# Kernel tuning notes

Measured on AMD Instinct MI355X. Metric: run time of the kernel, lower is better.

## Reference

```python
import jax, jax.numpy as jnp
import numpy as np

N_EXPERTS = 8
D_MODEL = 1024
D_FF = 2048
N_TOKENS = 4096
TOP_K = 2


def _init_expert_weight(key, shape):
    # matches torch init: bound = sqrt(3) * (sqrt(1/3)/sqrt(fan_in)) = 1/sqrt(fan_in)
    fan_in = shape[1]
    bound = 1.0 / np.sqrt(fan_in)
    return jax.random.uniform(key, shape, dtype=jnp.float32, minval=-bound, maxval=bound)


def setup_inputs() -> dict:
    key = jax.random.key(0)
    k_x, k_idx, k_w, k1, k2, k3 = jax.random.split(key, 6)
    x = jax.random.normal(k_x, (N_TOKENS, D_MODEL), dtype=jnp.float32)
    expert_indices = jax.random.randint(k_idx, (N_TOKENS, TOP_K), 0, N_EXPERTS)
    expert_weights = jax.random.uniform(k_w, (N_TOKENS, TOP_K), dtype=jnp.float32)
    w1 = _init_expert_weight(k1, (N_EXPERTS, D_MODEL, D_FF))
    w2 = _init_expert_weight(k2, (N_EXPERTS, D_MODEL, D_FF))
    w3 = _init_expert_weight(k3, (N_EXPERTS, D_FF, D_MODEL))
    return {"x": x, "expert_indices": expert_indices, "expert_weights": expert_weights,
            "w1": w1, "w2": w2, "w3": w3}


def reference(x, expert_indices, expert_weights, w1, w2, w3):
    # SwiGLU per expert, computed densely over all (token, expert) pairs,
    # then the top-k selected expert outputs are gathered and combined.
    # Mathematically identical to the padded-bmm dispatch/combine in the source.
    gate = jax.nn.silu(jnp.einsum('td,edf->tef', x, w1))   # [T, E, F]
    value = jnp.einsum('td,edf->tef', x, w2)               # [T, E, F]
    hidden = gate * value                                  # [T, E, F]
    out_e = jnp.einsum('tef,efd->ted', hidden, w3)         # [T, E, D]
    # gather each token's top-k expert outputs: [T, K, D]
    sel = jnp.take_along_axis(out_e, expert_indices[:, :, None], axis=1)
    return jnp.sum(sel * expert_weights[:, :, None], axis=1)  # [T, D]
```

## Files before the change

kernel.cpp:

```cpp
#include <hip/hip_runtime.h>
#include <hip/hip_bf16.h>

#define N_TOK   4096
#define DM      1024
#define DF      2048
#define NEXP    8
#define NPAIR   (N_TOK * 2)
#define BM      128
#define BN      128
#define BK      32

typedef __attribute__((ext_vector_type(8))) short bf16x8;
typedef __attribute__((ext_vector_type(4))) float f32x4;

__device__ __forceinline__ unsigned short to_bf16(float f) {
    unsigned u = __builtin_bit_cast(unsigned, f);
    unsigned r = (u + 0x7FFFu + ((u >> 16) & 1u)) >> 16;
    return (unsigned short)r;
}
__device__ __forceinline__ unsigned pk_bf16(float a, float b) {
    return (unsigned)to_bf16(a) | ((unsigned)to_bf16(b) << 16);
}
__device__ __forceinline__ void gld16(const unsigned short* g, unsigned short* l) {
    __builtin_amdgcn_global_load_lds(
        (const __attribute__((address_space(1))) unsigned int*)(g),
        (__attribute__((address_space(3))) unsigned int*)(l), 16, 0, 0);
}

__global__ __launch_bounds__(1024)
void k_sort(const int* __restrict__ eidx, int* __restrict__ meta,
            int* __restrict__ rows) {
    __shared__ int cnt[NEXP];
    __shared__ int cur[NEXP];
    const int tid = threadIdx.x;
    if (tid < NEXP) cnt[tid] = 0;
    __syncthreads();
    #pragma unroll
    for (int i = tid; i < NPAIR; i += 1024) atomicAdd(&cnt[eidx[i] & 7], 1);
    __syncthreads();
    if (tid == 0) {
        int off = 0, mt = 0;
        for (int e = 0; e < NEXP; ++e) {
            meta[16 + e] = off; meta[25 + e] = mt; cur[e] = off;
            int c = cnt[e];
            off += c; mt += (c + BM - 1) / BM;
        }
        meta[16 + NEXP] = off; meta[25 + NEXP] = mt; meta[34] = mt;
    }
    __syncthreads();
    #pragma unroll
    for (int i = tid; i < NPAIR; i += 1024) {
        int e = eidx[i] & 7;
        int p = atomicAdd(&cur[e], 1);
        rows[p] = i;
    }
}

__device__ __forceinline__ void d_transpose(const float* __restrict__ src,
                                            unsigned short* __restrict__ dst,
                                            int K, int F, int e, int bx, int by,
                                            unsigned short* tile, int t) {
    const int k0 = by * 64;
    const int f0 = bx * 64;
    const float* s = src + (size_t)e * K * F;
    unsigned short* d = dst + (size_t)e * K * F;
    const int fi = t & 63;
    const int kg = t >> 6;
    #pragma unroll
    for (int i = 0; i < 16; ++i) {
        int k = kg * 16 + i;
        tile[k * 80 + fi] = to_bf16(s[(size_t)(k0 + k) * F + f0 + fi]);
    }
    __syncthreads();
    const int kc = (t & 7) * 8;
    const int fo = t >> 3;
    #pragma unroll
    for (int j = 0; j < 2; ++j) {
        int f = fo + j * 32;
        unsigned short v[8];
        #pragma unroll
        for (int i = 0; i < 8; ++i) v[i] = tile[(kc + i) * 80 + f];
        uint4 w;
        w.x = (unsigned)v[0] | ((unsigned)v[1] << 16);
        w.y = (unsigned)v[2] | ((unsigned)v[3] << 16);
        w.z = (unsigned)v[4] | ((unsigned)v[5] << 16);
        w.w = (unsigned)v[6] | ((unsigned)v[7] << 16);
        *(uint4*)&d[(size_t)(f0 + f) * K + k0 + kc] = w;
    }
}

__global__ __launch_bounds__(256)
void k_prepass(const float* __restrict__ x, unsigned short* __restrict__ xb,
               const float* __restrict__ w1, unsigned short* __restrict__ w1t,
               const float* __restrict__ w2, unsigned short* __restrict__ w2t,
               const float* __restrict__ w3, unsigned short* __restrict__ w3t) {
    __shared__ __align__(16) unsigned short tile[64 * 80];
    const int b = blockIdx.x;
    const int t = threadIdx.x;
    if (b < 2048) {
        int i = (b * 256 + t) * 8;
        float4 v0 = *(const float4*)(x + i);
        float4 v1 = *(const float4*)(x + i + 4);
        uint4 w;
        w.x = pk_bf16(v0.x, v0.y); w.y = pk_bf16(v0.z, v0.w);
        w.z = pk_bf16(v1.x, v1.y); w.w = pk_bf16(v1.z, v1.w);
        *(uint4*)(xb + i) = w;
    } else if (b < 6144) {
        int l = b - 2048;
        int e = l >> 9, rem = l & 511;
        d_transpose(w1, w1t, DM, DF, e, rem & 31, rem >> 5, tile, t);
    } else if (b < 10240) {
        int l = b - 6144;
        int e = l >> 9, rem = l & 511;
        d_transpose(w2, w2t, DM, DF, e, rem & 31, rem >> 5, tile, t);
    } else {
        int l = b - 10240;
        int e = l >> 9, rem = l & 511;
        d_transpose(w3, w3t, DF, DM, e, rem & 15, rem >> 4, tile, t);
    }
}

__device__ __forceinline__ bool xcd_map(const int* meta, int bid, int ngroups,
                                        int& mt, int& ng) {
    const int MT = meta[34];
    const int x = bid & 7;
    const int j = bid >> 3;
    const int q = MT >> 3, r = MT & 7;
    const int Sx = q + (x < r ? 1 : 0);
    if (Sx == 0 || j >= Sx * ngroups) return false;
    ng = j / Sx;
    const int mtl = j - ng * Sx;
    mt = x * q + (x < r ? x : r) + mtl;
    return true;
}

__global__ __launch_bounds__(256, 2)
void k_gemm1_bf(const unsigned short* __restrict__ xb,
                const unsigned short* __restrict__ w1t,
                const unsigned short* __restrict__ w2t,
                const int* __restrict__ meta,
                const int* __restrict__ rows,
                unsigned short* __restrict__ H)
{
    __shared__ __align__(16) unsigned short As [BM * BK];
    __shared__ __align__(16) unsigned short B1s[BN * BK];
    __shared__ __align__(16) unsigned short B2s[BN * BK];
    __shared__ int s_tok[BM];

    int mt, ng;
    if (!xcd_map(meta, blockIdx.x, DF / BN, mt, ng)) return;
    int e = 0;
    #pragma unroll
    for (int i = 0; i < NEXP - 1; ++i) if (mt >= meta[25 + i + 1]) e = i + 1;
    const int rowEnd = meta[16 + e + 1];
    const int row0   = meta[16 + e] + (mt - meta[25 + e]) * BM;
    const int f0     = ng * BN;
    const int tid    = threadIdx.x;

    if (tid < BM) {
        int gr = row0 + tid;
        s_tok[tid] = (gr < rowEnd) ? (rows[gr] >> 1) : 0;
    }
    __syncthreads();

    const int lane = tid & 63;
    const int wave = tid >> 6;
    const int r0 = wave * 32 + (lane >> 2);
    const int r1 = r0 + 16;
    const int kb = (lane & 3) * 8;
    const unsigned short* a_src0 = xb + (size_t)s_tok[r0] * DM + kb;
    const unsigned short* a_src1 = xb + (size_t)s_tok[r1] * DM + kb;
    const size_t wb = (size_t)e * DM * DF;
    const unsigned short* b1_src0 = w1t + wb + (size_t)(f0 + r0) * DM + kb;
    const unsigned short* b1_src1 = w1t + wb + (size_t)(f0 + r1) * DM + kb;
    const unsigned short* b2_src0 = w2t + wb + (size_t)(f0 + r0) * DM + kb;
    const unsigned short* b2_src1 = w2t + wb + (size_t)(f0 + r1) * DM + kb;
    unsigned short* As0  = &As [wave * 1024];
    unsigned short* As1  = &As [wave * 1024 + 512];
    unsigned short* B1s0 = &B1s[wave * 1024];
    unsigned short* B1s1 = &B1s[wave * 1024 + 512];
    unsigned short* B2s0 = &B2s[wave * 1024];
    unsigned short* B2s1 = &B2s[wave * 1024 + 512];

    f32x4 accg[4][4], accv[4][4];
    #pragma unroll
    for (int i = 0; i < 4; ++i)
        #pragma unroll
        for (int j = 0; j < 4; ++j) { accg[i][j] = (f32x4)0.f; accv[i][j] = (f32x4)0.f; }

    const int wm = (wave >> 1) * 64;
    const int wn = (wave & 1) * 64;
    const int am = lane & 15;
    const int ak = (lane >> 4) * 8;

    for (int k0 = 0; k0 < DM; k0 += BK) {
        gld16(a_src0 + k0, As0);
        gld16(a_src1 + k0, As1);
        gld16(b1_src0 + k0, B1s0);
        gld16(b1_src1 + k0, B1s1);
        gld16(b2_src0 + k0, B2s0);
        gld16(b2_src1 + k0, B2s1);
        __syncthreads();

        bf16x8 a[4], b1[4], b2[4];
        #pragma unroll
        for (int mi = 0; mi < 4; ++mi) a[mi] = *(const bf16x8*)&As[(wm + mi * 16 + am) * BK + ak];
        #pragma unroll
        for (int ni = 0; ni < 4; ++ni) {
            b1[ni] = *(const bf16x8*)&B1s[(wn + ni * 16 + am) * BK + ak];
            b2[ni] = *(const bf16x8*)&B2s[(wn + ni * 16 + am) * BK + ak];
        }
        #pragma unroll
        for (int mi = 0; mi < 4; ++mi)
            #pragma unroll
            for (int ni = 0; ni < 4; ++ni) {
                accg[mi][ni] = __builtin_amdgcn_mfma_f32_16x16x32_bf16(a[mi], b1[ni], accg[mi][ni], 0, 0, 0);
                accv[mi][ni] = __builtin_amdgcn_mfma_f32_16x16x32_bf16(a[mi], b2[ni], accv[mi][ni], 0, 0, 0);
            }
        __syncthreads();
    }

    const int cn = lane & 15;
    const int cq = (lane >> 4) * 4;
    #pragma unroll
    for (int mi = 0; mi < 4; ++mi) {
        #pragma unroll
        for (int r = 0; r < 4; ++r) {
            const int row = wm + mi * 16 + cq + r;
            const int gr  = row0 + row;
            if (gr < rowEnd) {
                unsigned short* dst = H + (size_t)gr * DF + f0 + wn;
                #pragma unroll
                for (int ni = 0; ni < 4; ++ni) {
                    float g = accg[mi][ni][r];
                    float v = accv[mi][ni][r];
                    float h = (g * v) / (1.f + __expf(-g));
                    dst[ni * 16 + cn] = to_bf16(h);
                }
            }
        }
    }
}

__global__ __launch_bounds__(256, 2)
void k_gemm2_bf(const unsigned short* __restrict__ H,
                const unsigned short* __restrict__ w3t,
                const int* __restrict__ meta,
                const int* __restrict__ rows,
                const float* __restrict__ ew,
                float* __restrict__ out)
{
    __shared__ __align__(16) unsigned short As[BM * BK];
    __shared__ __align__(16) unsigned short Bs[BN * BK];
    __shared__ int   s_tok[BM];
    __shared__ float s_w[BM];

    int mt, ng;
    if (!xcd_map(meta, blockIdx.x, DM / BN, mt, ng)) return;
    int e = 0;
    #pragma unroll
    for (int i = 0; i < NEXP - 1; ++i) if (mt >= meta[25 + i + 1]) e = i + 1;
    const int rowEnd = meta[16 + e + 1];
    const int row0   = meta[16 + e] + (mt - meta[25 + e]) * BM;
    const int d0     = ng * BN;
    const int tid    = threadIdx.x;

    if (tid < BM) {
        int gr = row0 + tid;
        if (gr < rowEnd) { int pr = rows[gr]; s_tok[tid] = pr >> 1; s_w[tid] = ew[pr]; }
        else             { s_tok[tid] = 0;    s_w[tid] = 0.f; }
    }
    __syncthreads();

    const int lane = tid & 63;
    const int wave = tid >> 6;
    const int r0 = wave * 32 + (lane >> 2);
    const int r1 = r0 + 16;
    const int kb = (lane & 3) * 8;
    int gr0 = row0 + r0; if (gr0 > NPAIR - 1) gr0 = NPAIR - 1;
    int gr1 = row0 + r1; if (gr1 > NPAIR - 1) gr1 = NPAIR - 1;
    const unsigned short* a_src0 = H + (size_t)gr0 * DF + kb;
    const unsigned short* a_src1 = H + (size_t)gr1 * DF + kb;
    const size_t wb = (size_t)e * DM * DF;
    const unsigned short* b_src0 = w3t + wb + (size_t)(d0 + r0) * DF + kb;
    const unsigned short* b_src1 = w3t + wb + (size_t)(d0 + r1) * DF + kb;
    unsigned short* As0 = &As[wave * 1024];
    unsigned short* As1 = &As[wave * 1024 + 512];
    unsigned short* Bs0 = &Bs[wave * 1024];
    unsigned short* Bs1 = &Bs[wave * 1024 + 512];

    f32x4 acc[4][4];
    #pragma unroll
    for (int i = 0; i < 4; ++i)
        #pragma unroll
        for (int j = 0; j < 4; ++j) acc[i][j] = (f32x4)0.f;

    const int wm = (wave >> 1) * 64;
    const int wn = (wave & 1) * 64;
    const int am = lane & 15;
    const int ak = (lane >> 4) * 8;

    for (int k0 = 0; k0 < DF; k0 += BK) {
        gld16(a_src0 + k0, As0);
        gld16(a_src1 + k0, As1);
        gld16(b_src0 + k0, Bs0);
        gld16(b_src1 + k0, Bs1);
        __syncthreads();

        bf16x8 a[4], b[4];
        #pragma unroll
        for (int mi = 0; mi < 4; ++mi) a[mi] = *(const bf16x8*)&As[(wm + mi * 16 + am) * BK + ak];
        #pragma unroll
        for (int ni = 0; ni < 4; ++ni) b[ni] = *(const bf16x8*)&Bs[(wn + ni * 16 + am) * BK + ak];
        #pragma unroll
        for (int mi = 0; mi < 4; ++mi)
            #pragma unroll
            for (int ni = 0; ni < 4; ++ni)
                acc[mi][ni] = __builtin_amdgcn_mfma_f32_16x16x32_bf16(a[mi], b[ni], acc[mi][ni], 0, 0, 0);
        __syncthreads();
    }

    const int cn = lane & 15;
    const int cq = (lane >> 4) * 4;
    #pragma unroll
    for (int mi = 0; mi < 4; ++mi) {
        #pragma unroll
        for (int r = 0; r < 4; ++r) {
            const int row = wm + mi * 16 + cq + r;
            const int gr  = row0 + row;
            if (gr < rowEnd) {
                const int   tok = s_tok[row];
                const float wgt = s_w[row];
                float* dst = out + (size_t)tok * DM + d0 + wn;
                #pragma unroll
                for (int ni = 0; ni < 4; ++ni)
                    atomicAdd(&dst[ni * 16 + cn], wgt * acc[mi][ni][r]);
            }
        }
    }
}

__global__ __launch_bounds__(256)
void k_fallback(const float* __restrict__ x, const int* __restrict__ eidx,
                const float* __restrict__ ew, const float* __restrict__ w1,
                const float* __restrict__ w2, const float* __restrict__ w3,
                float* __restrict__ out)
{
    __shared__ float xs[DM];
    __shared__ float hs[DF];
    const int pair = blockIdx.x;
    const int t = pair >> 1;
    const int e = eidx[pair] & 7;
    const float wgt = ew[pair];
    const int tid = threadIdx.x;
    for (int i = tid; i < DM; i += 256) xs[i] = x[(size_t)t * DM + i];
    __syncthreads();
    for (int f = tid; f < DF; f += 256) {
        const float* c1 = w1 + (size_t)e * DM * DF + f;
        const float* c2 = w2 + (size_t)e * DM * DF + f;
        float g = 0.f, v = 0.f;
        for (int d = 0; d < DM; ++d) {
            float xv = xs[d];
            g += xv * c1[(size_t)d * DF];
            v += xv * c2[(size_t)d * DF];
        }
        hs[f] = (g * v) / (1.f + __expf(-g));
    }
    __syncthreads();
    for (int d = tid; d < DM; d += 256) {
        const float* c3 = w3 + (size_t)e * DF * DM + d;
        float o = 0.f;
        for (int f = 0; f < DF; ++f) o += hs[f] * c3[(size_t)f * DM];
        atomicAdd(&out[(size_t)t * DM + d], wgt * o);
    }
}

extern "C" void kernel_launch(void* const* d_in, const int* in_sizes, int n_in,
                              void* d_out, int out_size, void* d_ws, size_t ws_size,
                              hipStream_t stream)
{
    const float* x  = (const float*)d_in[0];
    const int*   ei = (const int*)  d_in[1];
    const float* ew = (const float*)d_in[2];
    const float* w1 = (const float*)d_in[3];
    const float* w2 = (const float*)d_in[4];
    const float* w3 = (const float*)d_in[5];
    float* out = (float*)d_out;

    (void)hipMemsetAsync(d_out, 0, (size_t)out_size * sizeof(float), stream);

    const size_t SZ_H  = (size_t)NPAIR * DF * 2;
    const size_t SZ_XB = (size_t)N_TOK * DM * 2;
    const size_t SZ_W  = (size_t)NEXP * DM * DF * 2;
    const size_t OFF_H  = 65536;
    const size_t OFF_XB = OFF_H + SZ_H;
    const size_t OFF_W1 = OFF_XB + SZ_XB;
    const size_t OFF_W2 = OFF_W1 + SZ_W;
    const size_t OFF_W3 = OFF_W2 + SZ_W;
    const size_t NEED_BIG = OFF_W3 + SZ_W;

    if (ws_size < NEED_BIG) {
        k_fallback<<<NPAIR, 256, 0, stream>>>(x, ei, ew, w1, w2, w3, out);
        return;
    }

    int* meta = (int*)d_ws;
    int* rows = meta + 64;
    unsigned short* H   = (unsigned short*)((char*)d_ws + OFF_H);
    unsigned short* xb  = (unsigned short*)((char*)d_ws + OFF_XB);
    unsigned short* w1t = (unsigned short*)((char*)d_ws + OFF_W1);
    unsigned short* w2t = (unsigned short*)((char*)d_ws + OFF_W2);
    unsigned short* w3t = (unsigned short*)((char*)d_ws + OFF_W3);

    k_sort<<<1, 1024, 0, stream>>>(ei, meta, rows);
    k_prepass<<<14336, 256, 0, stream>>>(x, xb, w1, w1t, w2, w2t, w3, w3t);

    k_gemm1_bf<<<1152, 256, 0, stream>>>(xb, w1t, w2t, meta, rows, H);
    k_gemm2_bf<<<640, 256, 0, stream>>>(H, w3t, meta, rows, ew, out);
}
```

Baseline: 419.0 us.

## Replace atomic scatter-add with per-pair staging buffer and combine kernel

The second GEMM now writes weighted per-pair outputs to a dense staging buffer (reusing the w1t region, which is dead by then) instead of doing atomicAdd into the output. A new combine kernel sums each token's two rows using a recorded position map, which also removes the output memset. Both GEMMs also drop the XCD-aware block remapping in favour of a plain 2D grid. The change trades atomic contention for an extra 32MB write and read pass plus one more launch, and the simpler grid may lose L2 locality across XCDs.

```diff
diff --git a/kernel.cpp b/kernel.cpp
--- a/kernel.cpp
+++ b/kernel.cpp
@@ -29,7 +29,7 @@
 
 __global__ __launch_bounds__(1024)
 void k_sort(const int* __restrict__ eidx, int* __restrict__ meta,
-            int* __restrict__ rows) {
+            int* __restrict__ rows, int* __restrict__ pos) {
     __shared__ int cnt[NEXP];
     __shared__ int cur[NEXP];
     const int tid = threadIdx.x;
@@ -53,6 +53,7 @@
         int e = eidx[i] & 7;
         int p = atomicAdd(&cur[e], 1);
         rows[p] = i;
+        pos[i]  = p;
     }
 }
 
@@ -120,20 +121,6 @@
     }
 }
 
-__device__ __forceinline__ bool xcd_map(const int* meta, int bid, int ngroups,
-                                        int& mt, int& ng) {
-    const int MT = meta[34];
-    const int x = bid & 7;
-    const int j = bid >> 3;
-    const int q = MT >> 3, r = MT & 7;
-    const int Sx = q + (x < r ? 1 : 0);
-    if (Sx == 0 || j >= Sx * ngroups) return false;
-    ng = j / Sx;
-    const int mtl = j - ng * Sx;
-    mt = x * q + (x < r ? x : r) + mtl;
-    return true;
-}
-
 __global__ __launch_bounds__(256, 2)
 void k_gemm1_bf(const unsigned short* __restrict__ xb,
                 const unsigned short* __restrict__ w1t,
@@ -147,14 +134,14 @@
     __shared__ __align__(16) unsigned short B2s[BN * BK];
     __shared__ int s_tok[BM];
 
-    int mt, ng;
-    if (!xcd_map(meta, blockIdx.x, DF / BN, mt, ng)) return;
+    const int mt = blockIdx.y;
+    if (mt >= meta[34]) return;
     int e = 0;
     #pragma unroll
     for (int i = 0; i < NEXP - 1; ++i) if (mt >= meta[25 + i + 1]) e = i + 1;
     const int rowEnd = meta[16 + e + 1];
     const int row0   = meta[16 + e] + (mt - meta[25 + e]) * BM;
-    const int f0     = ng * BN;
+    const int f0     = blockIdx.x * BN;
     const int tid    = threadIdx.x;
 
     if (tid < BM) {
@@ -248,21 +235,21 @@
                 const int* __restrict__ meta,
                 const int* __restrict__ rows,
                 const float* __restrict__ ew,
-                float* __restrict__ out)
+                float* __restrict__ S)
 {
     __shared__ __align__(16) unsigned short As[BM * BK];
     __shared__ __align__(16) unsigned short Bs[BN * BK];
     __shared__ int   s_tok[BM];
     __shared__ float s_w[BM];
 
-    int mt, ng;
-    if (!xcd_map(meta, blockIdx.x, DM / BN, mt, ng)) return;
+    const int mt = blockIdx.y;
+    if (mt >= meta[34]) return;
     int e = 0;
     #pragma unroll
     for (int i = 0; i < NEXP - 1; ++i) if (mt >= meta[25 + i + 1]) e = i + 1;
     const int rowEnd = meta[16 + e + 1];
     const int row0   = meta[16 + e] + (mt - meta[25 + e]) * BM;
-    const int d0     = ng * BN;
+    const int d0     = blockIdx.x * BN;
     const int tid    = threadIdx.x;
 
     if (tid < BM) {
@@ -329,15 +316,29 @@
             const int row = wm + mi * 16 + cq + r;
             const int gr  = row0 + row;
             if (gr < rowEnd) {
-                const int   tok = s_tok[row];
                 const float wgt = s_w[row];
-                float* dst = out + (size_t)tok * DM + d0 + wn;
+                float* dst = S + (size_t)gr * DM + d0 + wn;
                 #pragma unroll
                 for (int ni = 0; ni < 4; ++ni)
-                    atomicAdd(&dst[ni * 16 + cn], wgt * acc[mi][ni][r]);
+                    dst[ni * 16 + cn] = wgt * acc[mi][ni][r];
             }
         }
     }
+}
+
+__global__ __launch_bounds__(256)
+void k_combine(const float* __restrict__ S, const int* __restrict__ pos,
+               float* __restrict__ out) {
+    const int idx = blockIdx.x * 256 + threadIdx.x;
+    const int t   = idx >> 8;
+    const int d4  = idx & 255;
+    const int p0 = pos[2 * t];
+    const int p1 = pos[2 * t + 1];
+    const float4 a = *(const float4*)(S + (size_t)p0 * DM + d4 * 4);
+    const float4 b = *(const float4*)(S + (size_t)p1 * DM + d4 * 4);
+    float4 o;
+    o.x = a.x + b.x; o.y = a.y + b.y; o.z = a.z + b.z; o.w = a.w + b.w;
+    *(float4*)(out + (size_t)t * DM + d4 * 4) = o;
 }
 
 __global__ __launch_bounds__(256)
@@ -387,12 +388,10 @@
     const float* w3 = (const float*)d_in[5];
     float* out = (float*)d_out;
 
-    (void)hipMemsetAsync(d_out, 0, (size_t)out_size * sizeof(float), stream);
-
     const size_t SZ_H  = (size_t)NPAIR * DF * 2;
     const size_t SZ_XB = (size_t)N_TOK * DM * 2;
     const size_t SZ_W  = (size_t)NEXP * DM * DF * 2;
-    const size_t OFF_H  = 65536;
+    const size_t OFF_H  = 131072;
     const size_t OFF_XB = OFF_H + SZ_H;
     const size_t OFF_W1 = OFF_XB + SZ_XB;
     const size_t OFF_W2 = OFF_W1 + SZ_W;
@@ -400,21 +399,26 @@
     const size_t NEED_BIG = OFF_W3 + SZ_W;
 
     if (ws_size < NEED_BIG) {
+        (void)hipMemsetAsync(d_out, 0, (size_t)out_size * sizeof(float), stream);
         k_fallback<<<NPAIR, 256, 0, stream>>>(x, ei, ew, w1, w2, w3, out);
         return;
     }
 
     int* meta = (int*)d_ws;
     int* rows = meta + 64;
+    int* pos  = rows + NPAIR;
     unsigned short* H   = (unsigned short*)((char*)d_ws + OFF_H);
     unsigned short* xb  = (unsigned short*)((char*)d_ws + OFF_XB);
     unsigned short* w1t = (unsigned short*)((char*)d_ws + OFF_W1);
     unsigned short* w2t = (unsigned short*)((char*)d_ws + OFF_W2);
     unsigned short* w3t = (unsigned short*)((char*)d_ws + OFF_W3);
-
-    k_sort<<<1, 1024, 0, stream>>>(ei, meta, rows);
+    float* S = (float*)((char*)d_ws + OFF_W1);
+
+    k_sort<<<1, 1024, 0, stream>>>(ei, meta, rows, pos);
     k_prepass<<<14336, 256, 0, stream>>>(x, xb, w1, w1t, w2, w2t, w3, w3t);
 
-    k_gemm1_bf<<<1152, 256, 0, stream>>>(xb, w1t, w2t, meta, rows, H);
-    k_gemm2_bf<<<640, 256, 0, stream>>>(H, w3t, meta, rows, ew, out);
-}
+    const int NMT = NPAIR / BM + NEXP;
+    k_gemm1_bf<<<dim3(DF / BN, NMT), 256, 0, stream>>>(xb, w1t, w2t, meta, rows, H);
+    k_gemm2_bf<<<dim3(DM / BN, NMT), 256, 0, stream>>>(H, w3t, meta, rows, ew, S);
+    k_combine<<<(N_TOK * DM / 4) / 256, 256, 0, stream>>>(S, pos, out);
+}
```

New measurement: 407.3 us. 2.8% less time.
